# Performance work log

Hardware: AMD Instinct MI355X
Metric: run time of the kernel (lower is better)

## Reference

```python
import jax, jax.numpy as jnp
import numpy as np

BATCH = 16384
MAX_ACTIVE = 32
FEAT = 768
HIDDEN = 1024


def setup_inputs() -> dict:
    key = jax.random.key(0)
    k1, k2, k3, k4, k5, k6 = jax.random.split(key, 6)
    stm = jax.random.randint(k1, (BATCH, MAX_ACTIVE), 0, FEAT, dtype=jnp.int32)
    nstm = jax.random.randint(k2, (BATCH, MAX_ACTIVE), 0, FEAT, dtype=jnp.int32)
    # Linear params (PyTorch layout: weight is (out_features, in_features))
    ft_w = jax.random.normal(k3, (HIDDEN, FEAT), dtype=jnp.float32) * 0.05
    ft_b = jax.random.normal(k4, (HIDDEN,), dtype=jnp.float32) * 0.05
    out_w = jax.random.normal(k5, (1, 2 * HIDDEN), dtype=jnp.float32) * 0.05
    out_b = jax.random.normal(k6, (1,), dtype=jnp.float32) * 0.05
    return {"stm": stm, "nstm": nstm, "ft_w": ft_w, "ft_b": ft_b,
            "out_w": out_w, "out_b": out_b}


def sparse_to_dense(indices: jnp.ndarray, size: int = FEAT) -> jnp.ndarray:
    """(B, max_active) int indices with -1 padding -> (B, size) 0/1 float32."""
    b = indices.shape[0]
    valid = (indices >= 0).astype(jnp.float32)          # (B, A)
    cols = jnp.clip(indices, 0, size - 1)               # padded -> col 0, masked by `valid`
    rows = jnp.arange(b, dtype=jnp.int32)[:, None]      # (B, 1) broadcast
    dense = jnp.zeros((b, size), dtype=jnp.float32)
    # .max matches torch's set-to-1 semantics even if duplicate indices occur
    return dense.at[rows, cols].max(valid)


def reference(stm, nstm, ft_w, ft_b, out_w, out_b):
    stm_d = sparse_to_dense(stm)                        # (B, 768)
    nstm_d = sparse_to_dense(nstm)                      # (B, 768)
    stm_h = stm_d @ ft_w.T + ft_b                       # (B, H)
    nstm_h = nstm_d @ ft_w.T + ft_b                     # (B, H)
    hidden = jnp.concatenate([stm_h, nstm_h], axis=1)   # (B, 2H)
    hidden = jnp.clip(hidden, 0.0, 1.0)
    return jax.nn.sigmoid(hidden @ out_w.T + out_b)     # (B, 1)
```

## Files before the change

kernel.cpp:

```cpp
#include <hip/hip_runtime.h>
#include <stdint.h>

#define BATCH 16384
#define MAXA 32
#define FEAT 768
#define HIDDEN 1024

__global__ __launch_bounds__(256) void prep_quant(const float* __restrict__ ftw,
                                                  uint8_t* __restrict__ wQ,
                                                  float* __restrict__ scale) {
  const int h0 = blockIdx.x * 8;
  const int hloc = threadIdx.x >> 5;
  const int l32 = threadIdx.x & 31;
  const int h = h0 + hloc;

  float w[24];
  float amax = 0.f;
  const float* __restrict__ src = ftw + (size_t)h * FEAT;
#pragma unroll
  for (int k = 0; k < 24; ++k) {
    w[k] = src[l32 + 32 * k];
    amax = fmaxf(amax, fabsf(w[k]));
  }
#pragma unroll
  for (int m = 1; m <= 16; m <<= 1)
    amax = fmaxf(amax, __shfl_xor(amax, m, 64));
  amax = fmaxf(amax, 1e-20f);
  if (l32 == 0) scale[h] = amax / 127.f;
  const float inv = 127.f / amax;

  __shared__ __align__(16) uint8_t tile[FEAT * 8];
#pragma unroll
  for (int k = 0; k < 24; ++k) {
    int q = __float2int_rn(w[k] * inv);
    tile[(l32 + 32 * k) * 8 + hloc] = (uint8_t)(q + 128);
  }
  __syncthreads();

#pragma unroll
  for (int p = 0; p < 3; ++p) {
    int f = threadIdx.x + 256 * p;
    unsigned long long v = *(const unsigned long long*)&tile[f * 8];
    *(unsigned long long*)(wQ + (size_t)f * HIDDEN + h0) = v;
  }

  if (blockIdx.x == 0)
    ((uint32_t*)(wQ + (size_t)FEAT * HIDDEN))[threadIdx.x] = 0x80808080u;
}

__device__ __forceinline__ void acc16(uint32_t* acc, uint4 w) {
  acc[0] += __builtin_amdgcn_perm(0u, w.x, 0x0c010c00u);
  acc[1] += __builtin_amdgcn_perm(0u, w.x, 0x0c030c02u);
  acc[2] += __builtin_amdgcn_perm(0u, w.y, 0x0c010c00u);
  acc[3] += __builtin_amdgcn_perm(0u, w.y, 0x0c030c02u);
  acc[4] += __builtin_amdgcn_perm(0u, w.z, 0x0c010c00u);
  acc[5] += __builtin_amdgcn_perm(0u, w.z, 0x0c030c02u);
  acc[6] += __builtin_amdgcn_perm(0u, w.w, 0x0c010c00u);
  acc[7] += __builtin_amdgcn_perm(0u, w.w, 0x0c030c02u);
}

__global__ __launch_bounds__(256) void nn_fwd(
    const int* __restrict__ stm, const int* __restrict__ nstm,
    const uint8_t* __restrict__ wQ, const float* __restrict__ scale,
    const float* __restrict__ bias, const float* __restrict__ outw,
    const float* __restrict__ outb, float* __restrict__ out)
{
  const int lane = threadIdx.x & 63;
  const int wid  = threadIdx.x >> 6;
  const int rsel = wid >> 1;
  const int side = wid & 1;
  const int row  = blockIdx.x * 2 + rsel;
  const int pos  = lane & 31;

  const int* __restrict__ src = side ? nstm : stm;
  int idx = src[row * MAXA + pos];
  bool valid = idx >= 0;
#pragma unroll
  for (int j = 0; j < 31; ++j) {
    int other = __shfl(idx, j, 64);
    if (j < pos && other == idx) valid = false;
  }
  const int fmap = valid ? idx : FEAT;

  uint32_t acc[8];
#pragma unroll
  for (int k = 0; k < 8; ++k) acc[k] = 0u;

#pragma unroll
  for (int j = 0; j < 32; ++j) {
    int f_ = __builtin_amdgcn_readlane(fmap, j);
    uint4 w_ = ((const uint4*)(wQ + (size_t)f_ * HIDDEN))[lane];
    acc16(acc, w_);
  }

  const int DB = 32 * 128;

  const int hbase = lane * 16;
  const float4* s4 = (const float4*)(scale + hbase);
  const float4* b4 = (const float4*)(bias + hbase);
  const float4* o4 = (const float4*)(outw + side * HIDDEN + hbase);
  float partial = 0.f;
#pragma unroll
  for (int q = 0; q < 4; ++q) {
    float4 s = s4[q], b = b4[q], o = o4[q];
    uint32_t a0 = acc[2 * q], a1 = acc[2 * q + 1];
    int q0 = (int)(a0 & 0xffffu) - DB;
    int q1 = (int)(a0 >> 16)    - DB;
    int q2 = (int)(a1 & 0xffffu) - DB;
    int q3 = (int)(a1 >> 16)    - DB;
    float h0 = fminf(fmaxf(fmaf((float)q0, s.x, b.x), 0.f), 1.f);
    float h1 = fminf(fmaxf(fmaf((float)q1, s.y, b.y), 0.f), 1.f);
    float h2 = fminf(fmaxf(fmaf((float)q2, s.z, b.z), 0.f), 1.f);
    float h3 = fminf(fmaxf(fmaf((float)q3, s.w, b.w), 0.f), 1.f);
    partial += h0 * o.x + h1 * o.y + h2 * o.z + h3 * o.w;
  }
#pragma unroll
  for (int off = 32; off > 0; off >>= 1)
    partial += __shfl_down(partial, off, 64);

  __shared__ float lpart[2];
  if (side == 1 && lane == 0) lpart[rsel] = partial;
  __syncthreads();
  if (side == 0 && lane == 0) {
    float y = partial + lpart[rsel] + outb[0];
    out[row] = 1.f / (1.f + __expf(-y));
  }
}

extern "C" void kernel_launch(void* const* d_in, const int* in_sizes, int n_in,
                              void* d_out, int out_size, void* d_ws, size_t ws_size,
                              hipStream_t stream) {
  const int*   stm  = (const int*)d_in[0];
  const int*   nstm = (const int*)d_in[1];
  const float* ftw  = (const float*)d_in[2];
  const float* ftb  = (const float*)d_in[3];
  const float* outw = (const float*)d_in[4];
  const float* outb = (const float*)d_in[5];

  uint8_t* wQ    = (uint8_t*)d_ws;
  float*   scale = (float*)(wQ + (size_t)(FEAT + 1) * HIDDEN);

  prep_quant<<<HIDDEN / 8, 256, 0, stream>>>(ftw, wQ, scale);
  nn_fwd<<<BATCH / 2, 256, 0, stream>>>(stm, nstm, wQ, scale, ftb, outw, outb,
                                        (float*)d_out);
}
```

Before: 123.9 us.

## Stream quantized weight chunks through double-buffered LDS shared by 32 rows

Each block now handles 32 rows (both sides) with 512 threads. It streams the int8 weight table through LDS in 64-feature chunks using a register-staged double buffer. Active features are gathered from LDS per phase via ballot masks, where before each row gathered directly from global/L2. Invalid slots are skipped and the bias offset is corrected by the per-row valid count. This trades global gather traffic for a full weight sweep per block (768KB per 32 rows), heavy register use (64 accumulators) and many barriers.

```diff
diff --git a/kernel.cpp b/kernel.cpp
--- a/kernel.cpp
+++ b/kernel.cpp
@@ -5,6 +5,12 @@
 #define MAXA 32
 #define FEAT 768
 #define HIDDEN 1024
+
+#define CHUNK 64
+#define NPHASE (FEAT / CHUNK)
+#define CBYTES (CHUNK * HIDDEN)
+#define THREADS 512
+#define ROWS_PB 32
 
 __global__ __launch_bounds__(256) void prep_quant(const float* __restrict__ ftw,
                                                   uint8_t* __restrict__ wQ,
@@ -43,9 +49,6 @@
     unsigned long long v = *(const unsigned long long*)&tile[f * 8];
     *(unsigned long long*)(wQ + (size_t)f * HIDDEN + h0) = v;
   }
-
-  if (blockIdx.x == 0)
-    ((uint32_t*)(wQ + (size_t)FEAT * HIDDEN))[threadIdx.x] = 0x80808080u;
 }
 
 __device__ __forceinline__ void acc16(uint32_t* acc, uint4 w) {
@@ -59,71 +62,129 @@
   acc[7] += __builtin_amdgcn_perm(0u, w.w, 0x0c030c02u);
 }
 
-__global__ __launch_bounds__(256) void nn_fwd(
+__global__ __launch_bounds__(THREADS) void nn_fwd(
     const int* __restrict__ stm, const int* __restrict__ nstm,
     const uint8_t* __restrict__ wQ, const float* __restrict__ scale,
     const float* __restrict__ bias, const float* __restrict__ outw,
     const float* __restrict__ outb, float* __restrict__ out)
 {
-  const int lane = threadIdx.x & 63;
-  const int wid  = threadIdx.x >> 6;
-  const int rsel = wid >> 1;
-  const int side = wid & 1;
-  const int row  = blockIdx.x * 2 + rsel;
+  const int tid  = threadIdx.x;
+  const int lane = tid & 63;
+  const int wv   = tid >> 6;
   const int pos  = lane & 31;
-
-  const int* __restrict__ src = side ? nstm : stm;
-  int idx = src[row * MAXA + pos];
-  bool valid = idx >= 0;
-#pragma unroll
-  for (int j = 0; j < 31; ++j) {
-    int other = __shfl(idx, j, 64);
-    if (j < pos && other == idx) valid = false;
-  }
-  const int fmap = valid ? idx : FEAT;
-
-  uint32_t acc[8];
-#pragma unroll
-  for (int k = 0; k < 8; ++k) acc[k] = 0u;
-
-#pragma unroll
-  for (int j = 0; j < 32; ++j) {
-    int f_ = __builtin_amdgcn_readlane(fmap, j);
-    uint4 w_ = ((const uint4*)(wQ + (size_t)f_ * HIDDEN))[lane];
-    acc16(acc, w_);
-  }
-
-  const int DB = 32 * 128;
+  const int row0 = blockIdx.x * ROWS_PB;
+
+  __shared__ __align__(16) uint8_t lds[2][CBYTES];
+
+  int fmap[8]; int nval[8];
+#pragma unroll
+  for (int k = 0; k < 8; ++k) {
+    const int r = row0 + wv * 4 + (k >> 1);
+    const int* __restrict__ s = (k & 1) ? nstm : stm;
+    int idx = s[r * MAXA + pos];
+    bool valid = idx >= 0;
+#pragma unroll
+    for (int j = 0; j < 31; ++j) {
+      int other = __shfl(idx, j, 64);
+      if (j < pos && other == idx) valid = false;
+    }
+    unsigned long long b = __ballot(valid);
+    nval[k] = __builtin_popcount((uint32_t)b);
+    fmap[k] = valid ? idx : 4096;
+  }
+
+  uint32_t accs[8][8];
+#pragma unroll
+  for (int k = 0; k < 8; ++k)
+#pragma unroll
+    for (int i = 0; i < 8; ++i) accs[k][i] = 0u;
+
+  uint4 stv[8];
+  {
+    const uint4* g = (const uint4*)wQ;
+#pragma unroll
+    for (int s = 0; s < 8; ++s) stv[s] = g[tid + (s << 9)];
+    uint4* d = (uint4*)lds[0];
+#pragma unroll
+    for (int s = 0; s < 8; ++s) d[tid + (s << 9)] = stv[s];
+  }
+  __syncthreads();
+
+  for (int p = 0; p < NPHASE; ++p) {
+    if (p + 1 < NPHASE) {
+      const uint4* g = (const uint4*)(wQ + (size_t)(p + 1) * CBYTES);
+#pragma unroll
+      for (int s = 0; s < 8; ++s) stv[s] = g[tid + (s << 9)];
+    }
+
+    const uint8_t* buf = lds[p & 1];
+    uint32_t mk[8];
+#pragma unroll
+    for (int k = 0; k < 8; ++k)
+      mk[k] = (uint32_t)__ballot((fmap[k] >> 6) == p);
+    uint32_t any = mk[0]|mk[1]|mk[2]|mk[3]|mk[4]|mk[5]|mk[6]|mk[7];
+
+    while (any) {
+      uint4 v[8];
+      int have = 0;
+#pragma unroll
+      for (int k = 0; k < 8; ++k) {
+        if (mk[k]) {
+          int j = __builtin_ctz(mk[k]); mk[k] &= mk[k] - 1;
+          int f = __builtin_amdgcn_readlane(fmap[k], j);
+          v[k] = *(const uint4*)(buf + ((f & (CHUNK - 1)) << 10) + (lane << 4));
+          have |= 1 << k;
+        }
+      }
+#pragma unroll
+      for (int k = 0; k < 8; ++k)
+        if (have & (1 << k)) acc16(accs[k], v[k]);
+      any = mk[0]|mk[1]|mk[2]|mk[3]|mk[4]|mk[5]|mk[6]|mk[7];
+    }
+
+    if (p + 1 < NPHASE) {
+      uint4* d = (uint4*)lds[(p + 1) & 1];
+#pragma unroll
+      for (int s = 0; s < 8; ++s) d[tid + (s << 9)] = stv[s];
+    }
+    __syncthreads();
+  }
 
   const int hbase = lane * 16;
-  const float4* s4 = (const float4*)(scale + hbase);
-  const float4* b4 = (const float4*)(bias + hbase);
-  const float4* o4 = (const float4*)(outw + side * HIDDEN + hbase);
-  float partial = 0.f;
-#pragma unroll
-  for (int q = 0; q < 4; ++q) {
-    float4 s = s4[q], b = b4[q], o = o4[q];
-    uint32_t a0 = acc[2 * q], a1 = acc[2 * q + 1];
-    int q0 = (int)(a0 & 0xffffu) - DB;
-    int q1 = (int)(a0 >> 16)    - DB;
-    int q2 = (int)(a1 & 0xffffu) - DB;
-    int q3 = (int)(a1 >> 16)    - DB;
-    float h0 = fminf(fmaxf(fmaf((float)q0, s.x, b.x), 0.f), 1.f);
-    float h1 = fminf(fmaxf(fmaf((float)q1, s.y, b.y), 0.f), 1.f);
-    float h2 = fminf(fmaxf(fmaf((float)q2, s.z, b.z), 0.f), 1.f);
-    float h3 = fminf(fmaxf(fmaf((float)q3, s.w, b.w), 0.f), 1.f);
-    partial += h0 * o.x + h1 * o.y + h2 * o.z + h3 * o.w;
-  }
-#pragma unroll
-  for (int off = 32; off > 0; off >>= 1)
-    partial += __shfl_down(partial, off, 64);
-
-  __shared__ float lpart[2];
-  if (side == 1 && lane == 0) lpart[rsel] = partial;
-  __syncthreads();
-  if (side == 0 && lane == 0) {
-    float y = partial + lpart[rsel] + outb[0];
-    out[row] = 1.f / (1.f + __expf(-y));
+  float part[8];
+#pragma unroll
+  for (int k = 0; k < 8; ++k) {
+    const int DB = 128 * nval[k];
+    const float4* s4 = (const float4*)(scale + hbase);
+    const float4* b4 = (const float4*)(bias + hbase);
+    const float4* o4 = (const float4*)(outw + (k & 1) * HIDDEN + hbase);
+    float partial = 0.f;
+#pragma unroll
+    for (int q = 0; q < 4; ++q) {
+      float4 s = s4[q], b = b4[q], o = o4[q];
+      uint32_t a0 = accs[k][2 * q], a1 = accs[k][2 * q + 1];
+      int q0 = (int)(a0 & 0xffffu) - DB;
+      int q1 = (int)(a0 >> 16)    - DB;
+      int q2 = (int)(a1 & 0xffffu) - DB;
+      int q3 = (int)(a1 >> 16)    - DB;
+      float h0 = fminf(fmaxf(fmaf((float)q0, s.x, b.x), 0.f), 1.f);
+      float h1 = fminf(fmaxf(fmaf((float)q1, s.y, b.y), 0.f), 1.f);
+      float h2 = fminf(fmaxf(fmaf((float)q2, s.z, b.z), 0.f), 1.f);
+      float h3 = fminf(fmaxf(fmaf((float)q3, s.w, b.w), 0.f), 1.f);
+      partial += h0 * o.x + h1 * o.y + h2 * o.z + h3 * o.w;
+    }
+#pragma unroll
+    for (int off = 32; off > 0; off >>= 1)
+      partial += __shfl_down(partial, off, 64);
+    part[k] = partial;
+  }
+  if (lane == 0) {
+    const float ob = outb[0];
+#pragma unroll
+    for (int r2 = 0; r2 < 4; ++r2) {
+      float y = part[2 * r2] + part[2 * r2 + 1] + ob;
+      out[row0 + wv * 4 + r2] = 1.f / (1.f + __expf(-y));
+    }
   }
 }
 
@@ -141,6 +202,6 @@
   float*   scale = (float*)(wQ + (size_t)(FEAT + 1) * HIDDEN);
 
   prep_quant<<<HIDDEN / 8, 256, 0, stream>>>(ftw, wQ, scale);
-  nn_fwd<<<BATCH / 2, 256, 0, stream>>>(stm, nstm, wQ, scale, ftb, outw, outb,
-                                        (float*)d_out);
-}
+  nn_fwd<<<BATCH / ROWS_PB, THREADS, 0, stream>>>(stm, nstm, wQ, scale, ftb,
+                                                  outw, outb, (float*)d_out);
+}
```

Result: slower. 222.4 us (+79.6%).

## Stage hidden-dim weight slices in LDS and split rows across slice blocks

Applied to the files above, without the earlier changes.

Replaces the per-row gather from global memory with blocks that each copy a 128-column slice of the quantized weight table (about 98KB) into shared memory. Each block then serves 128 batch rows, gathering from LDS and accumulating partial output dot products with float atomics. A separate finish kernel applies the bias and sigmoid. This is meant to cut repeated global/L2 gather traffic. In exchange it adds a third launch, atomics, redundant index loading and dedup in every slice block, and large LDS use that limits occupancy.

```diff
diff --git a/kernel.cpp b/kernel.cpp
--- a/kernel.cpp
+++ b/kernel.cpp
@@ -6,9 +6,16 @@
 #define FEAT 768
 #define HIDDEN 1024
 
+#define SLICE_H 128
+#define NSLICE (HIDDEN / SLICE_H)
+#define ROWS_PB 128
+#define RS_PB (ROWS_PB * 2)
+#define THREADS 512
+
 __global__ __launch_bounds__(256) void prep_quant(const float* __restrict__ ftw,
                                                   uint8_t* __restrict__ wQ,
-                                                  float* __restrict__ scale) {
+                                                  float* __restrict__ scale,
+                                                  float* __restrict__ opart) {
   const int h0 = blockIdx.x * 8;
   const int hloc = threadIdx.x >> 5;
   const int l32 = threadIdx.x & 31;
@@ -46,6 +53,8 @@
 
   if (blockIdx.x == 0)
     ((uint32_t*)(wQ + (size_t)FEAT * HIDDEN))[threadIdx.x] = 0x80808080u;
+  if (blockIdx.x < 64)
+    opart[blockIdx.x * 256 + threadIdx.x] = 0.f;
 }
 
 __device__ __forceinline__ void acc16(uint32_t* acc, uint4 w) {
@@ -59,72 +68,119 @@
   acc[7] += __builtin_amdgcn_perm(0u, w.w, 0x0c030c02u);
 }
 
-__global__ __launch_bounds__(256) void nn_fwd(
+__global__ __launch_bounds__(THREADS) void nn_slice(
     const int* __restrict__ stm, const int* __restrict__ nstm,
     const uint8_t* __restrict__ wQ, const float* __restrict__ scale,
     const float* __restrict__ bias, const float* __restrict__ outw,
-    const float* __restrict__ outb, float* __restrict__ out)
+    float* __restrict__ opart)
 {
-  const int lane = threadIdx.x & 63;
-  const int wid  = threadIdx.x >> 6;
-  const int rsel = wid >> 1;
-  const int side = wid & 1;
-  const int row  = blockIdx.x * 2 + rsel;
-  const int pos  = lane & 31;
-
-  const int* __restrict__ src = side ? nstm : stm;
-  int idx = src[row * MAXA + pos];
-  bool valid = idx >= 0;
-#pragma unroll
-  for (int j = 0; j < 31; ++j) {
-    int other = __shfl(idx, j, 64);
-    if (j < pos && other == idx) valid = false;
-  }
-  const int fmap = valid ? idx : FEAT;
-
-  uint32_t acc[8];
-#pragma unroll
-  for (int k = 0; k < 8; ++k) acc[k] = 0u;
-
-#pragma unroll
-  for (int j = 0; j < 32; ++j) {
-    int f_ = __builtin_amdgcn_readlane(fmap, j);
-    uint4 w_ = ((const uint4*)(wQ + (size_t)f_ * HIDDEN))[lane];
-    acc16(acc, w_);
-  }
-
+  const int tid   = threadIdx.x;
+  const int lane  = tid & 63;
+  const int wv    = tid >> 6;
+  const int slice = blockIdx.x & (NSLICE - 1);
+  const int row0  = (blockIdx.x >> 3) * ROWS_PB;
+  const int half  = lane >> 5;
+  const int pos   = lane & 31;
+  const int g     = lane >> 3;
+  const int i8    = lane & 7;
+
+  __shared__ __align__(16) uint8_t  sl[(FEAT + 1) * SLICE_H];
+  __shared__ __align__(16) uint16_t fl[RS_PB * 32];
+
+  int idxA[16];
+#pragma unroll
+  for (int it = 0; it < 16; ++it) {
+    int row = row0 + wv * 16 + it;
+    const int* __restrict__ s = half ? nstm : stm;
+    idxA[it] = s[row * MAXA + pos];
+  }
+#pragma unroll
+  for (int it = 0; it < 16; ++it) {
+    int rs  = wv * 32 + it * 2 + half;
+    int idx = idxA[it];
+    bool valid = idx >= 0;
+#pragma unroll
+    for (int j = 0; j < 31; ++j) {
+      int other = __shfl(idx, (half << 5) | j, 64);
+      if (j < pos && other == idx) valid = false;
+    }
+    fl[rs * 32 + pos] = (uint16_t)(valid ? idx : FEAT);
+  }
+
+#pragma unroll
+  for (int p = 0; p < 12; ++p) {
+    int f = p * 64 + (tid >> 3);
+    uint4 v = *(const uint4*)(wQ + (size_t)f * HIDDEN + slice * SLICE_H + i8 * 16);
+    *(uint4*)(sl + f * SLICE_H + i8 * 16) = v;
+  }
+  if (tid < 8) {
+    uint4 v = *(const uint4*)(wQ + (size_t)FEAT * HIDDEN + slice * SLICE_H + tid * 16);
+    *(uint4*)(sl + FEAT * SLICE_H + tid * 16) = v;
+  }
+  __syncthreads();
+
+  const int i16base = i8 * 16;
   const int DB = 32 * 128;
 
-  const int hbase = lane * 16;
-  const float4* s4 = (const float4*)(scale + hbase);
-  const float4* b4 = (const float4*)(bias + hbase);
-  const float4* o4 = (const float4*)(outw + side * HIDDEN + hbase);
-  float partial = 0.f;
-#pragma unroll
-  for (int q = 0; q < 4; ++q) {
-    float4 s = s4[q], b = b4[q], o = o4[q];
-    uint32_t a0 = acc[2 * q], a1 = acc[2 * q + 1];
-    int q0 = (int)(a0 & 0xffffu) - DB;
-    int q1 = (int)(a0 >> 16)    - DB;
-    int q2 = (int)(a1 & 0xffffu) - DB;
-    int q3 = (int)(a1 >> 16)    - DB;
-    float h0 = fminf(fmaxf(fmaf((float)q0, s.x, b.x), 0.f), 1.f);
-    float h1 = fminf(fmaxf(fmaf((float)q1, s.y, b.y), 0.f), 1.f);
-    float h2 = fminf(fmaxf(fmaf((float)q2, s.z, b.z), 0.f), 1.f);
-    float h3 = fminf(fmaxf(fmaf((float)q3, s.w, b.w), 0.f), 1.f);
-    partial += h0 * o.x + h1 * o.y + h2 * o.z + h3 * o.w;
-  }
-#pragma unroll
-  for (int off = 32; off > 0; off >>= 1)
-    partial += __shfl_down(partial, off, 64);
-
-  __shared__ float lpart[2];
-  if (side == 1 && lane == 0) lpart[rsel] = partial;
-  __syncthreads();
-  if (side == 0 && lane == 0) {
-    float y = partial + lpart[rsel] + outb[0];
-    out[row] = 1.f / (1.f + __expf(-y));
-  }
+#pragma unroll 1
+  for (int p = 0; p < 4; ++p) {
+    const int rs = wv * 32 + p * 8 + g;
+
+    uint32_t l[16];
+    {
+      const uint4* lp = (const uint4*)(fl + rs * 32);
+      uint4 a = lp[0], b = lp[1], c = lp[2], d = lp[3];
+      l[0]=a.x; l[1]=a.y; l[2]=a.z; l[3]=a.w;
+      l[4]=b.x; l[5]=b.y; l[6]=b.z; l[7]=b.w;
+      l[8]=c.x; l[9]=c.y; l[10]=c.z; l[11]=c.w;
+      l[12]=d.x; l[13]=d.y; l[14]=d.z; l[15]=d.w;
+    }
+
+    uint32_t acc[8];
+#pragma unroll
+    for (int k = 0; k < 8; ++k) acc[k] = 0u;
+
+#pragma unroll
+    for (int j = 0; j < 32; ++j) {
+      uint32_t f = (j & 1) ? (l[j >> 1] >> 16) : (l[j >> 1] & 0xffffu);
+      uint4 v = *(const uint4*)(sl + f * SLICE_H + i16base);
+      acc16(acc, v);
+    }
+
+    const int hbase = slice * SLICE_H + i16base;
+    const float4* s4 = (const float4*)(scale + hbase);
+    const float4* b4 = (const float4*)(bias + hbase);
+    const float4* o4 = (const float4*)(outw + (rs & 1) * HIDDEN + hbase);
+    float partial = 0.f;
+#pragma unroll
+    for (int q = 0; q < 4; ++q) {
+      float4 s = s4[q], b = b4[q], o = o4[q];
+      uint32_t a0 = acc[2 * q], a1 = acc[2 * q + 1];
+      int q0 = (int)(a0 & 0xffffu) - DB;
+      int q1 = (int)(a0 >> 16)    - DB;
+      int q2 = (int)(a1 & 0xffffu) - DB;
+      int q3 = (int)(a1 >> 16)    - DB;
+      float h0 = fminf(fmaxf(fmaf((float)q0, s.x, b.x), 0.f), 1.f);
+      float h1 = fminf(fmaxf(fmaf((float)q1, s.y, b.y), 0.f), 1.f);
+      float h2 = fminf(fmaxf(fmaf((float)q2, s.z, b.z), 0.f), 1.f);
+      float h3 = fminf(fmaxf(fmaf((float)q3, s.w, b.w), 0.f), 1.f);
+      partial += h0 * o.x + h1 * o.y + h2 * o.z + h3 * o.w;
+    }
+    partial += __shfl_xor(partial, 1, 64);
+    partial += __shfl_xor(partial, 2, 64);
+    partial += __shfl_xor(partial, 4, 64);
+    partial += __shfl_xor(partial, 8, 64);
+    if ((lane & 15) == 0)
+      atomicAdd(&opart[row0 + (rs >> 1)], partial);
+  }
+}
+
+__global__ __launch_bounds__(256) void nn_finish(const float* __restrict__ opart,
+                                                 const float* __restrict__ outb,
+                                                 float* __restrict__ out) {
+  const int i = blockIdx.x * 256 + threadIdx.x;
+  float y = opart[i] + outb[0];
+  out[i] = 1.f / (1.f + __expf(-y));
 }
 
 extern "C" void kernel_launch(void* const* d_in, const int* in_sizes, int n_in,
@@ -139,8 +195,10 @@
 
   uint8_t* wQ    = (uint8_t*)d_ws;
   float*   scale = (float*)(wQ + (size_t)(FEAT + 1) * HIDDEN);
-
-  prep_quant<<<HIDDEN / 8, 256, 0, stream>>>(ftw, wQ, scale);
-  nn_fwd<<<BATCH / 2, 256, 0, stream>>>(stm, nstm, wQ, scale, ftb, outw, outb,
-                                        (float*)d_out);
-}
+  float*   opart = scale + HIDDEN;
+
+  prep_quant<<<HIDDEN / 8, 256, 0, stream>>>(ftw, wQ, scale, opart);
+  nn_slice<<<(BATCH / ROWS_PB) * NSLICE, THREADS, 0, stream>>>(
+      stm, nstm, wQ, scale, ftb, outw, opart);
+  nn_finish<<<BATCH / 256, 256, 0, stream>>>(opart, outb, (float*)d_out);
+}
```

New measurement: 194.8 us. 1.57x slower.

## Process two rows and both perspectives per wavefront to amortize epilogue

Applied to the files above, without the earlier changes.

Each wavefront now handles two batch rows and both the stm and nstm sides, keeping four accumulator sets, instead of one row-side per wavefront. Scale, bias and output-weight loads and the dequant epilogue are amortized across four accumulations, and the shared-memory exchange and __syncthreads between waves are removed. The gather loop issues four independent loads per iteration for more memory-level parallelism. In exchange, register pressure roughly quadruples for accumulators, which may lower occupancy, and the grid shrinks by a factor of four.

```diff
diff --git a/kernel.cpp b/kernel.cpp
--- a/kernel.cpp
+++ b/kernel.cpp
@@ -59,6 +59,11 @@
   acc[7] += __builtin_amdgcn_perm(0u, w.w, 0x0c030c02u);
 }
 
+__device__ __forceinline__ float dq(uint32_t a, int hi, float s, float b) {
+  int q = (int)(hi ? (a >> 16) : (a & 0xffffu)) - 32 * 128;
+  return fminf(fmaxf(fmaf((float)q, s, b), 0.f), 1.f);
+}
+
 __global__ __launch_bounds__(256) void nn_fwd(
     const int* __restrict__ stm, const int* __restrict__ nstm,
     const uint8_t* __restrict__ wQ, const float* __restrict__ scale,
@@ -67,63 +72,77 @@
 {
   const int lane = threadIdx.x & 63;
   const int wid  = threadIdx.x >> 6;
-  const int rsel = wid >> 1;
-  const int side = wid & 1;
-  const int row  = blockIdx.x * 2 + rsel;
+  const int rowA = blockIdx.x * 8 + wid * 2;
+  const int rowB = rowA + 1;
+  const int half = lane >> 5;
   const int pos  = lane & 31;
 
-  const int* __restrict__ src = side ? nstm : stm;
-  int idx = src[row * MAXA + pos];
-  bool valid = idx >= 0;
+  const int* __restrict__ src = half ? nstm : stm;
+  int idxA = src[rowA * MAXA + pos];
+  int idxB = src[rowB * MAXA + pos];
+  bool vA = idxA >= 0, vB = idxB >= 0;
 #pragma unroll
   for (int j = 0; j < 31; ++j) {
-    int other = __shfl(idx, j, 64);
-    if (j < pos && other == idx) valid = false;
+    int oA = __shfl(idxA, (half << 5) | j, 64);
+    int oB = __shfl(idxB, (half << 5) | j, 64);
+    if (j < pos && oA == idxA) vA = false;
+    if (j < pos && oB == idxB) vB = false;
   }
-  const int fmap = valid ? idx : FEAT;
+  const int fmA = vA ? idxA : FEAT;
+  const int fmB = vB ? idxB : FEAT;
 
-  uint32_t acc[8];
+  uint32_t aAs[8], aAn[8], aBs[8], aBn[8];
 #pragma unroll
-  for (int k = 0; k < 8; ++k) acc[k] = 0u;
+  for (int k = 0; k < 8; ++k) { aAs[k] = 0u; aAn[k] = 0u; aBs[k] = 0u; aBn[k] = 0u; }
 
 #pragma unroll
   for (int j = 0; j < 32; ++j) {
-    int f_ = __builtin_amdgcn_readlane(fmap, j);
-    uint4 w_ = ((const uint4*)(wQ + (size_t)f_ * HIDDEN))[lane];
-    acc16(acc, w_);
+    int fAs = __builtin_amdgcn_readlane(fmA, j);
+    int fAn = __builtin_amdgcn_readlane(fmA, 32 + j);
+    int fBs = __builtin_amdgcn_readlane(fmB, j);
+    int fBn = __builtin_amdgcn_readlane(fmB, 32 + j);
+    uint4 wAs = ((const uint4*)(wQ + (size_t)fAs * HIDDEN))[lane];
+    uint4 wAn = ((const uint4*)(wQ + (size_t)fAn * HIDDEN))[lane];
+    uint4 wBs = ((const uint4*)(wQ + (size_t)fBs * HIDDEN))[lane];
+    uint4 wBn = ((const uint4*)(wQ + (size_t)fBn * HIDDEN))[lane];
+    acc16(aAs, wAs);
+    acc16(aAn, wAn);
+    acc16(aBs, wBs);
+    acc16(aBn, wBn);
   }
-
-  const int DB = 32 * 128;
 
   const int hbase = lane * 16;
   const float4* s4 = (const float4*)(scale + hbase);
   const float4* b4 = (const float4*)(bias + hbase);
-  const float4* o4 = (const float4*)(outw + side * HIDDEN + hbase);
-  float partial = 0.f;
+  const float4* oS4 = (const float4*)(outw + hbase);
+  const float4* oN4 = (const float4*)(outw + HIDDEN + hbase);
+  float pA = 0.f, pB = 0.f;
 #pragma unroll
   for (int q = 0; q < 4; ++q) {
-    float4 s = s4[q], b = b4[q], o = o4[q];
-    uint32_t a0 = acc[2 * q], a1 = acc[2 * q + 1];
-    int q0 = (int)(a0 & 0xffffu) - DB;
-    int q1 = (int)(a0 >> 16)    - DB;
-    int q2 = (int)(a1 & 0xffffu) - DB;
-    int q3 = (int)(a1 >> 16)    - DB;
-    float h0 = fminf(fmaxf(fmaf((float)q0, s.x, b.x), 0.f), 1.f);
-    float h1 = fminf(fmaxf(fmaf((float)q1, s.y, b.y), 0.f), 1.f);
-    float h2 = fminf(fmaxf(fmaf((float)q2, s.z, b.z), 0.f), 1.f);
-    float h3 = fminf(fmaxf(fmaf((float)q3, s.w, b.w), 0.f), 1.f);
-    partial += h0 * o.x + h1 * o.y + h2 * o.z + h3 * o.w;
+    float4 s = s4[q], b = b4[q], oS = oS4[q], oN = oN4[q];
+    uint32_t a0, a1;
+    a0 = aAs[2 * q]; a1 = aAs[2 * q + 1];
+    pA += dq(a0, 0, s.x, b.x) * oS.x + dq(a0, 1, s.y, b.y) * oS.y +
+          dq(a1, 0, s.z, b.z) * oS.z + dq(a1, 1, s.w, b.w) * oS.w;
+    a0 = aAn[2 * q]; a1 = aAn[2 * q + 1];
+    pA += dq(a0, 0, s.x, b.x) * oN.x + dq(a0, 1, s.y, b.y) * oN.y +
+          dq(a1, 0, s.z, b.z) * oN.z + dq(a1, 1, s.w, b.w) * oN.w;
+    a0 = aBs[2 * q]; a1 = aBs[2 * q + 1];
+    pB += dq(a0, 0, s.x, b.x) * oS.x + dq(a0, 1, s.y, b.y) * oS.y +
+          dq(a1, 0, s.z, b.z) * oS.z + dq(a1, 1, s.w, b.w) * oS.w;
+    a0 = aBn[2 * q]; a1 = aBn[2 * q + 1];
+    pB += dq(a0, 0, s.x, b.x) * oN.x + dq(a0, 1, s.y, b.y) * oN.y +
+          dq(a1, 0, s.z, b.z) * oN.z + dq(a1, 1, s.w, b.w) * oN.w;
   }
 #pragma unroll
-  for (int off = 32; off > 0; off >>= 1)
-    partial += __shfl_down(partial, off, 64);
-
-  __shared__ float lpart[2];
-  if (side == 1 && lane == 0) lpart[rsel] = partial;
-  __syncthreads();
-  if (side == 0 && lane == 0) {
-    float y = partial + lpart[rsel] + outb[0];
-    out[row] = 1.f / (1.f + __expf(-y));
+  for (int off = 32; off > 0; off >>= 1) {
+    pA += __shfl_down(pA, off, 64);
+    pB += __shfl_down(pB, off, 64);
+  }
+  if (lane == 0) {
+    const float ob = outb[0];
+    out[rowA] = 1.f / (1.f + __expf(-(pA + ob)));
+    out[rowB] = 1.f / (1.f + __expf(-(pB + ob)));
   }
 }
 
@@ -141,6 +160,6 @@
   float*   scale = (float*)(wQ + (size_t)(FEAT + 1) * HIDDEN);
 
   prep_quant<<<HIDDEN / 8, 256, 0, stream>>>(ftw, wQ, scale);
-  nn_fwd<<<BATCH / 2, 256, 0, stream>>>(stm, nstm, wQ, scale, ftb, outw, outb,
+  nn_fwd<<<BATCH / 8, 256, 0, stream>>>(stm, nstm, wQ, scale, ftb, outw, outb,
                                         (float*)d_out);
 }
```

Measured after the change: 112.8 us, median of 2. 9.0% less time.
